# Kernel optimization log

Hardware: AMD Instinct MI355X
Metric: run time of the kernel (lower is better)

## Reference

```python
import jax, jax.numpy as jnp
import numpy as np

B, H, S, D = 2, 12, 2048, 64
N_GLOBAL = 128


def setup_inputs() -> dict:
    key = jax.random.key(0)
    kq, kk, kv = jax.random.split(key, 3)
    q = jax.random.normal(kq, (B, H, S, D), dtype=jnp.float32)
    k = jax.random.normal(kk, (B, H, S, D), dtype=jnp.float32)
    v = jax.random.normal(kv, (B, H, S, D), dtype=jnp.float32)
    # first N_GLOBAL tokens of every sequence are global (CLS/special tokens)
    attention_mask = jnp.broadcast_to((jnp.arange(S) < N_GLOBAL).astype(jnp.int32), (B, S))
    return {"q": q, "k": k, "v": v, "attention_mask": attention_mask}


def reference(q, k, v, attention_mask):
    Bb, Hh, Ss, Dd = q.shape
    scale = jnp.sqrt(jnp.float32(Dd))
    is_global = attention_mask > 0                      # [B, S]
    counts = is_global.sum(axis=1)                      # [B]
    # stable argsort puts global token indices first (matches per-row packing loop)
    order = jnp.argsort(~is_global, axis=1, stable=True)  # [B, S]
    valid = jnp.arange(Ss)[None, :] < counts[:, None]     # [B, S] slot < count
    idx = order[:, None, :, None]                          # [B,1,S,1]
    gk = jnp.where(valid[:, None, :, None],
                   jnp.take_along_axis(k, idx, axis=2), 0.0)  # packed global_k [B,H,S,D]
    gv = jnp.where(valid[:, None, :, None],
                   jnp.take_along_axis(v, idx, axis=2), 0.0)  # packed global_v
    # all-tokens -> global-tokens attention (padded global slots masked to -inf)
    scores = jnp.einsum('bhqd,bhgd->bhqg', q, gk) / scale
    scores = jnp.where(valid[:, None, None, :], scores, -jnp.inf)
    probs = jax.nn.softmax(scores.astype(jnp.float32), axis=-1)  # [B,H,S,S]
    context = jnp.einsum('bhqg,bhgd->bhqd', probs, gv)           # [B,H,S,D]
    # global tokens attend to everything; overwrite their rows (scatter in original)
    full_scores = jnp.einsum('bhqd,bhkd->bhqk', q, k) / scale
    full_probs = jax.nn.softmax(full_scores.astype(jnp.float32), axis=-1)
    ctx_full = jnp.einsum('bhqk,bhkd->bhqd', full_probs, v)
    context = jnp.where(is_global[:, None, :, None], ctx_full, context)
    return context, probs
```

## Files before the change

kernel.cpp:

```cpp
#include <hip/hip_runtime.h>
#include <math.h>


namespace {
constexpr int BATCH = 2;
constexpr int HEADS = 12;
constexpr int SEQ   = 2048;
constexpr int DIM   = 64;
constexpr int NG    = 128;
constexpr int BHN   = BATCH * HEADS;
constexpr long long CTX_SIZE = (long long)BHN * SEQ * DIM;
constexpr float SCALE = 0.125f;

constexpr int NB_BLOCKS = (BHN * NG) / 16;
constexpr int NA_BLOCKS = (BHN * SEQ) / 16;
constexpr int NZ_BLOCKS = 6144;
constexpr int TAIL_F4   = (SEQ - NG) / 4;
}

typedef float nfloat4 __attribute__((ext_vector_type(4)));

__device__ __forceinline__ float wave_max64(float x) {
#pragma unroll
    for (int off = 32; off > 0; off >>= 1) x = fmaxf(x, __shfl_xor(x, off));
    return x;
}
__device__ __forceinline__ float wave_sum64(float x) {
#pragma unroll
    for (int off = 32; off > 0; off >>= 1) x += __shfl_xor(x, off);
    return x;
}

__global__ __launch_bounds__(256) void longformer_fused(
    const float* __restrict__ q, const float* __restrict__ k,
    const float* __restrict__ v, float* __restrict__ out)
{
    __shared__ float k_lds[128][68];
    __shared__ float p_lds[4][4][128];

    const int blk = blockIdx.x;
    float* const ctx_out   = out;
    float* const probs_out = out + CTX_SIZE;

    if (blk >= NB_BLOCKS + NA_BLOCKS) {
        const unsigned tid    = (unsigned)(blk - NB_BLOCKS - NA_BLOCKS) * 256u + threadIdx.x;
        const unsigned stride = (unsigned)NZ_BLOCKS * 256u;
        const unsigned total  = (unsigned)(BHN * SEQ) * (unsigned)TAIL_F4;
        const nfloat4 z = (nfloat4)(0.f);
        for (unsigned i = tid; i < total; i += stride) {
            unsigned row = i / TAIL_F4;
            unsigned c4  = i - row * TAIL_F4;
            nfloat4* p = reinterpret_cast<nfloat4*>(probs_out + (size_t)row * SEQ + NG + 4u * c4);
            __builtin_nontemporal_store(z, p);
        }
        return;
    }

    const int w    = threadIdx.x >> 6;
    const int lane = threadIdx.x & 63;
    const int gq   = lane >> 4;
    const int dq   = lane & 15;

    if (blk >= NB_BLOCKS) {
        const int ablk  = blk - NB_BLOCKS;
        const int bh    = ablk >> 7;
        const int qbase = (ablk & 127) << 4;
        const int row0  = qbase + w * 4;
        const float* const qb = q + (size_t)bh * SEQ * DIM;
        const float* const kb = k + (size_t)bh * SEQ * DIM;
        const float* const vb = v + (size_t)bh * SEQ * DIM;

#pragma unroll
        for (int j = 0; j < 8; ++j) {
            int f  = threadIdx.x + j * 256;
            int g  = f >> 4;
            int ci = (f & 15) << 2;
            float4 t = *reinterpret_cast<const float4*>(kb + g * DIM + ci);
            *reinterpret_cast<float4*>(&k_lds[g][ci]) = t;
        }
        __syncthreads();

        float s0[4] = {0,0,0,0}, s1[4] = {0,0,0,0};
        const float* krow0 = &k_lds[lane][0];
        const float* krow1 = &k_lds[lane + 64][0];
#pragma unroll 4
        for (int i = 0; i < 16; ++i) {
            const float4 ka = *reinterpret_cast<const float4*>(krow0 + 4 * i);
            const float4 kc = *reinterpret_cast<const float4*>(krow1 + 4 * i);
#pragma unroll
            for (int r = 0; r < 4; ++r) {
                const float4 qv = *reinterpret_cast<const float4*>(qb + (size_t)(row0 + r) * DIM + 4 * i);
                s0[r] += qv.x * ka.x + qv.y * ka.y + qv.z * ka.z + qv.w * ka.w;
                s1[r] += qv.x * kc.x + qv.y * kc.y + qv.z * kc.z + qv.w * kc.w;
            }
        }
#pragma unroll
        for (int r = 0; r < 4; ++r) {
            float a = s0[r] * SCALE, b = s1[r] * SCALE;
            float m = wave_max64(fmaxf(a, b));
            float e0 = __expf(a - m), e1 = __expf(b - m);
            float inv = 1.f / wave_sum64(e0 + e1);
            e0 *= inv; e1 *= inv;
            p_lds[w][r][lane]      = e0;
            p_lds[w][r][lane + 64] = e1;
            float* prow = probs_out + (size_t)(bh * SEQ + row0 + r) * SEQ;
            __builtin_nontemporal_store(e0, prow + lane);
            __builtin_nontemporal_store(e1, prow + lane + 64);
        }
        __syncthreads();

        if (qbase >= NG) {
            float4 c[4];
#pragma unroll
            for (int r = 0; r < 4; ++r) c[r] = make_float4(0.f, 0.f, 0.f, 0.f);
#pragma unroll 2
            for (int i = 0; i < 32; ++i) {
                const int g = 4 * i + gq;
                const float4 vv = *reinterpret_cast<const float4*>(vb + g * DIM + 4 * dq);
#pragma unroll
                for (int r = 0; r < 4; ++r) {
                    const float pr = p_lds[w][r][g];
                    c[r].x += pr * vv.x; c[r].y += pr * vv.y;
                    c[r].z += pr * vv.z; c[r].w += pr * vv.w;
                }
            }
#pragma unroll
            for (int r = 0; r < 4; ++r) {
                c[r].x += __shfl_xor(c[r].x, 16); c[r].y += __shfl_xor(c[r].y, 16);
                c[r].z += __shfl_xor(c[r].z, 16); c[r].w += __shfl_xor(c[r].w, 16);
                c[r].x += __shfl_xor(c[r].x, 32); c[r].y += __shfl_xor(c[r].y, 32);
                c[r].z += __shfl_xor(c[r].z, 32); c[r].w += __shfl_xor(c[r].w, 32);
                if (lane < 16) {
                    nfloat4 cv; cv.x = c[r].x; cv.y = c[r].y; cv.z = c[r].z; cv.w = c[r].w;
                    nfloat4* crow = reinterpret_cast<nfloat4*>(ctx_out + (size_t)(bh * SEQ + row0 + r) * DIM + 4 * dq);
                    __builtin_nontemporal_store(cv, crow);
                }
            }
        }
        return;
    }

    {
        const int bh    = blk >> 3;
        const int qbase = (blk & 7) << 4;
        const int row0  = qbase + w * 4;
        const float* const qb = q + (size_t)bh * SEQ * DIM;
        const float* const kb = k + (size_t)bh * SEQ * DIM;
        const float* const vb = v + (size_t)bh * SEQ * DIM;

        float m[4], l[4];
        float4 c[4];
#pragma unroll
        for (int r = 0; r < 4; ++r) { m[r] = -INFINITY; l[r] = 0.f; c[r] = make_float4(0.f,0.f,0.f,0.f); }

        for (int t = 0; t < 16; ++t) {
            const float* kt = kb + (size_t)t * 128 * DIM;
            const float* vt = vb + (size_t)t * 128 * DIM;

            __syncthreads();
#pragma unroll
            for (int j = 0; j < 8; ++j) {
                int f  = threadIdx.x + j * 256;
                int g  = f >> 4;
                int ci = (f & 15) << 2;
                float4 tt = *reinterpret_cast<const float4*>(kt + g * DIM + ci);
                *reinterpret_cast<float4*>(&k_lds[g][ci]) = tt;
            }
            __syncthreads();

            float s0[4] = {0,0,0,0}, s1[4] = {0,0,0,0};
            const float* krow0 = &k_lds[lane][0];
            const float* krow1 = &k_lds[lane + 64][0];
#pragma unroll 4
            for (int i = 0; i < 16; ++i) {
                const float4 ka = *reinterpret_cast<const float4*>(krow0 + 4 * i);
                const float4 kc = *reinterpret_cast<const float4*>(krow1 + 4 * i);
#pragma unroll
                for (int r = 0; r < 4; ++r) {
                    const float4 qv = *reinterpret_cast<const float4*>(qb + (size_t)(row0 + r) * DIM + 4 * i);
                    s0[r] += qv.x * ka.x + qv.y * ka.y + qv.z * ka.z + qv.w * ka.w;
                    s1[r] += qv.x * kc.x + qv.y * kc.y + qv.z * kc.z + qv.w * kc.w;
                }
            }
#pragma unroll
            for (int r = 0; r < 4; ++r) {
                float a  = s0[r] * SCALE, b = s1[r] * SCALE;
                float tm = wave_max64(fmaxf(a, b));
                float mn = fmaxf(m[r], tm);
                float corr = __expf(m[r] - mn);
                float e0 = __expf(a - mn), e1 = __expf(b - mn);
                float ts = wave_sum64(e0 + e1);
                l[r] = l[r] * corr + ts;
                c[r].x *= corr; c[r].y *= corr; c[r].z *= corr; c[r].w *= corr;
                m[r] = mn;
                p_lds[w][r][lane]      = e0;
                p_lds[w][r][lane + 64] = e1;
            }
            __syncthreads();
#pragma unroll 2
            for (int i = 0; i < 32; ++i) {
                const int g = 4 * i + gq;
                const float4 vv = *reinterpret_cast<const float4*>(vt + g * DIM + 4 * dq);
#pragma unroll
                for (int r = 0; r < 4; ++r) {
                    const float pr = p_lds[w][r][g];
                    c[r].x += pr * vv.x; c[r].y += pr * vv.y;
                    c[r].z += pr * vv.z; c[r].w += pr * vv.w;
                }
            }
        }
#pragma unroll
        for (int r = 0; r < 4; ++r) {
            c[r].x += __shfl_xor(c[r].x, 16); c[r].y += __shfl_xor(c[r].y, 16);
            c[r].z += __shfl_xor(c[r].z, 16); c[r].w += __shfl_xor(c[r].w, 16);
            c[r].x += __shfl_xor(c[r].x, 32); c[r].y += __shfl_xor(c[r].y, 32);
            c[r].z += __shfl_xor(c[r].z, 32); c[r].w += __shfl_xor(c[r].w, 32);
            const float inv = 1.f / l[r];
            c[r].x *= inv; c[r].y *= inv; c[r].z *= inv; c[r].w *= inv;
            if (lane < 16) {
                nfloat4 cv; cv.x = c[r].x; cv.y = c[r].y; cv.z = c[r].z; cv.w = c[r].w;
                nfloat4* crow = reinterpret_cast<nfloat4*>(ctx_out + (size_t)(bh * SEQ + row0 + r) * DIM + 4 * dq);
                __builtin_nontemporal_store(cv, crow);
            }
        }
    }
}

extern "C" void kernel_launch(void* const* d_in, const int* in_sizes, int n_in,
                              void* d_out, int out_size, void* d_ws, size_t ws_size,
                              hipStream_t stream) {
    const float* q = (const float*)d_in[0];
    const float* k = (const float*)d_in[1];
    const float* v = (const float*)d_in[2];
    float* out = (float*)d_out;
    dim3 grid(NB_BLOCKS + NA_BLOCKS + NZ_BLOCKS);
    dim3 block(256);
    hipLaunchKernelGGL(longformer_fused, grid, block, 0, stream, q, k, v, out);
}
```

Baseline: 601.5 us.

## Fold probs tail zeroing into attention blocks and store P in fp16 LDS

Removes the separate zero-fill blocks and makes each all-to-global attention block write the zero tail of its own 16 probability rows, interleaved with the K tile load. The goal is to drop the extra blocks and their index math, and to overlap the large zero-store stream with compute. The probabilities staged in LDS for the P·V product are also stored as fp16 instead of fp32, halving LDS footprint and traffic. That lowers the precision of the context output (the probs output stays fp32), which could push results past tolerance.

```diff
diff --git a/kernel.cpp b/kernel.cpp
--- a/kernel.cpp
+++ b/kernel.cpp
@@ -1,4 +1,5 @@
 #include <hip/hip_runtime.h>
+#include <hip/hip_fp16.h>
 #include <math.h>
 
 
@@ -14,8 +15,8 @@
 
 constexpr int NB_BLOCKS = (BHN * NG) / 16;
 constexpr int NA_BLOCKS = (BHN * SEQ) / 16;
-constexpr int NZ_BLOCKS = 6144;
 constexpr int TAIL_F4   = (SEQ - NG) / 4;
+constexpr int TAIL_PER_THREAD = 16 * TAIL_F4 / 256;
 }
 
 typedef float nfloat4 __attribute__((ext_vector_type(4)));
@@ -35,26 +36,12 @@
     const float* __restrict__ q, const float* __restrict__ k,
     const float* __restrict__ v, float* __restrict__ out)
 {
-    __shared__ float k_lds[128][68];
-    __shared__ float p_lds[4][4][128];
+    __shared__ float  k_lds[128][68];
+    __shared__ __half p_lds[4][4][128];
 
     const int blk = blockIdx.x;
     float* const ctx_out   = out;
     float* const probs_out = out + CTX_SIZE;
-
-    if (blk >= NB_BLOCKS + NA_BLOCKS) {
-        const unsigned tid    = (unsigned)(blk - NB_BLOCKS - NA_BLOCKS) * 256u + threadIdx.x;
-        const unsigned stride = (unsigned)NZ_BLOCKS * 256u;
-        const unsigned total  = (unsigned)(BHN * SEQ) * (unsigned)TAIL_F4;
-        const nfloat4 z = (nfloat4)(0.f);
-        for (unsigned i = tid; i < total; i += stride) {
-            unsigned row = i / TAIL_F4;
-            unsigned c4  = i - row * TAIL_F4;
-            nfloat4* p = reinterpret_cast<nfloat4*>(probs_out + (size_t)row * SEQ + NG + 4u * c4);
-            __builtin_nontemporal_store(z, p);
-        }
-        return;
-    }
 
     const int w    = threadIdx.x >> 6;
     const int lane = threadIdx.x & 63;
@@ -78,6 +65,19 @@
             float4 t = *reinterpret_cast<const float4*>(kb + g * DIM + ci);
             *reinterpret_cast<float4*>(&k_lds[g][ci]) = t;
         }
+
+        {
+            float* const tail_base = probs_out + ((size_t)bh * SEQ + qbase) * SEQ;
+            const nfloat4 z = (nfloat4)(0.f);
+#pragma unroll
+            for (int s = 0; s < TAIL_PER_THREAD; ++s) {
+                int idx  = s * 256 + threadIdx.x;
+                int row  = idx / TAIL_F4;
+                int c4   = idx - row * TAIL_F4;
+                nfloat4* p = reinterpret_cast<nfloat4*>(tail_base + (size_t)row * SEQ + NG + 4 * c4);
+                __builtin_nontemporal_store(z, p);
+            }
+        }
         __syncthreads();
 
         float s0[4] = {0,0,0,0}, s1[4] = {0,0,0,0};
@@ -101,8 +101,8 @@
             float e0 = __expf(a - m), e1 = __expf(b - m);
             float inv = 1.f / wave_sum64(e0 + e1);
             e0 *= inv; e1 *= inv;
-            p_lds[w][r][lane]      = e0;
-            p_lds[w][r][lane + 64] = e1;
+            p_lds[w][r][lane]      = __float2half(e0);
+            p_lds[w][r][lane + 64] = __float2half(e1);
             float* prow = probs_out + (size_t)(bh * SEQ + row0 + r) * SEQ;
             __builtin_nontemporal_store(e0, prow + lane);
             __builtin_nontemporal_store(e1, prow + lane + 64);
@@ -119,7 +119,7 @@
                 const float4 vv = *reinterpret_cast<const float4*>(vb + g * DIM + 4 * dq);
 #pragma unroll
                 for (int r = 0; r < 4; ++r) {
-                    const float pr = p_lds[w][r][g];
+                    const float pr = __half2float(p_lds[w][r][g]);
                     c[r].x += pr * vv.x; c[r].y += pr * vv.y;
                     c[r].z += pr * vv.z; c[r].w += pr * vv.w;
                 }
@@ -193,8 +193,8 @@
                 l[r] = l[r] * corr + ts;
                 c[r].x *= corr; c[r].y *= corr; c[r].z *= corr; c[r].w *= corr;
                 m[r] = mn;
-                p_lds[w][r][lane]      = e0;
-                p_lds[w][r][lane + 64] = e1;
+                p_lds[w][r][lane]      = __float2half(e0);
+                p_lds[w][r][lane + 64] = __float2half(e1);
             }
             __syncthreads();
 #pragma unroll 2
@@ -203,7 +203,7 @@
                 const float4 vv = *reinterpret_cast<const float4*>(vt + g * DIM + 4 * dq);
 #pragma unroll
                 for (int r = 0; r < 4; ++r) {
-                    const float pr = p_lds[w][r][g];
+                    const float pr = __half2float(p_lds[w][r][g]);
                     c[r].x += pr * vv.x; c[r].y += pr * vv.y;
                     c[r].z += pr * vv.z; c[r].w += pr * vv.w;
                 }
@@ -233,7 +233,7 @@
     const float* k = (const float*)d_in[1];
     const float* v = (const float*)d_in[2];
     float* out = (float*)d_out;
-    dim3 grid(NB_BLOCKS + NA_BLOCKS + NZ_BLOCKS);
+    dim3 grid(NB_BLOCKS + NA_BLOCKS);
     dim3 block(256);
     hipLaunchKernelGGL(longformer_fused, grid, block, 0, stream, q, k, v, out);
 }
```

Measured after the change: 614.7 us. 1.02x slower.
